# Kernel optimization log

Hardware: AMD Instinct MI355X
Metric: run time of the kernel (lower is better)

## Reference

```python
import jax, jax.numpy as jnp
import numpy as np

NUM_CLASSES = 80
STRIDES = (8, 16, 32)
PRE_TOP_K = 1000
KEEP_TOP_K = 100
IOU_THR = 0.65
SCORE_THR = 0.25
CLASS_OFFSET = 8192.0  # > max image coordinate, separates classes for batched NMS


def _make_priors_strides(featmap_sizes):
    # MlvlPointGenerator.grid_priors with offset=0 (RTMDet-style point priors)
    priors, strides = [], []
    for (h, w), s in zip(featmap_sizes, STRIDES):
        ys, xs = jnp.meshgrid(jnp.arange(h, dtype=jnp.float32) * s,
                              jnp.arange(w, dtype=jnp.float32) * s, indexing='ij')
        priors.append(jnp.stack([xs.reshape(-1), ys.reshape(-1)], axis=-1))
        strides.append(jnp.full((h * w,), float(s), dtype=jnp.float32))
    return jnp.concatenate(priors, 0), jnp.concatenate(strides, 0)


def _flatten(x, c):
    # [B, C, H, W] -> [B, H*W, c] matching permute(0,2,3,1).reshape
    b = x.shape[0]
    return jnp.transpose(x, (0, 2, 3, 1)).reshape(b, -1, c)


def _iou_matrix(boxes):
    # boxes [K, 4] x1y1x2y2 -> pairwise IoU [K, K]
    area = jnp.maximum(boxes[:, 2] - boxes[:, 0], 0.0) * jnp.maximum(boxes[:, 3] - boxes[:, 1], 0.0)
    lt = jnp.maximum(boxes[:, None, :2], boxes[None, :, :2])
    rb = jnp.minimum(boxes[:, None, 2:], boxes[None, :, 2:])
    wh = jnp.maximum(rb - lt, 0.0)
    inter = wh[..., 0] * wh[..., 1]
    return inter / jnp.maximum(area[:, None] + area[None, :] - inter, 1e-6)


def _nms_single(boxes, scores, labels):
    # boxes [N,4], scores [N] (max over classes), labels [N] int32
    valid = scores > SCORE_THR
    scores = jnp.where(valid, scores, 0.0)
    top_scores, idx = jax.lax.top_k(scores, PRE_TOP_K)  # pre_top_k filtering
    b = boxes[idx]
    lab = labels[idx]
    val = valid[idx]
    # class-aware NMS via coordinate offset per class (batched_nms trick)
    off_boxes = b + (lab.astype(b.dtype) * CLASS_OFFSET)[:, None]
    iou = _iou_matrix(off_boxes)

    def body(suppressed, i):
        keep_i = ~suppressed[i]
        suppressed = suppressed | (keep_i & (iou[i] > IOU_THR))
        suppressed = suppressed.at[i].set(~keep_i)
        return suppressed, keep_i

    _, keeps = jax.lax.scan(body, ~val, jnp.arange(PRE_TOP_K))
    final_scores = jnp.where(keeps, top_scores, 0.0)
    fs, fidx = jax.lax.top_k(final_scores, KEEP_TOP_K)
    dets = jnp.concatenate([b[fidx], fs[:, None]], axis=-1)  # [keep_top_k, 5]
    return dets, lab[fidx]


def setup_inputs() -> dict:
    key = jax.random.key(0)
    ks = jax.random.split(key, 6)
    B, C = 16, NUM_CLASSES
    return {
        'cls0': jax.random.normal(ks[0], (B, C, 80, 80), jnp.float32),
        'cls1': jax.random.normal(ks[1], (B, C, 40, 40), jnp.float32),
        'cls2': jax.random.normal(ks[2], (B, C, 20, 20), jnp.float32),
        'box0': jax.random.uniform(ks[3], (B, 4, 80, 80), jnp.float32),
        'box1': jax.random.uniform(ks[4], (B, 4, 40, 40), jnp.float32),
        'box2': jax.random.uniform(ks[5], (B, 4, 20, 20), jnp.float32),
    }


def reference(cls0, cls1, cls2, box0, box1, box2):
    featmap_sizes = [c.shape[2:] for c in (cls0, cls1, cls2)]
    priors, strides = _make_priors_strides(featmap_sizes)  # [A,2], [A]
    scores = jax.nn.sigmoid(
        jnp.concatenate([_flatten(c, NUM_CLASSES) for c in (cls0, cls1, cls2)], axis=1))  # [B,A,C]
    preds = jnp.concatenate([_flatten(b, 4) for b in (box0, box1, box2)], axis=1)  # [B,A,4]
    # rtmdet_bbox_decoder: distances * stride around point priors
    d = preds * strides[None, :, None]
    x1 = priors[None, :, 0] - d[..., 0]
    y1 = priors[None, :, 1] - d[..., 1]
    x2 = priors[None, :, 0] + d[..., 2]
    y2 = priors[None, :, 1] + d[..., 3]
    bboxes = jnp.stack([x1, y1, x2, y2], axis=-1)  # [B,A,4]
    max_scores = jnp.max(scores, axis=-1)
    labels = jnp.argmax(scores, axis=-1).astype(jnp.int32)
    dets, out_labels = jax.vmap(_nms_single)(bboxes, max_scores, labels)
    return dets, out_labels
```

## Files before the change

### kernel.cpp

```cpp
#include <hip/hip_runtime.h>
#include <math.h>
#include <stdint.h>

typedef unsigned long long u64;
typedef unsigned int u32;

#define NCLS 80
#define NA   8400
#define NB   16
#define PRE_K 1000
#define M_FAST 256


__global__ __launch_bounds__(256) void k_decode(
    const float* __restrict__ cls0, const float* __restrict__ cls1,
    const float* __restrict__ cls2, const float* __restrict__ box0,
    const float* __restrict__ box1, const float* __restrict__ box2,
    u64* __restrict__ f_keys, float4* __restrict__ boxes,
    int* __restrict__ labels)
{
    int pa = blockIdx.x * 256 + threadIdx.x;
    int b  = blockIdx.y;
    if (pa >= 4200) return;

    const float *clsp, *boxp;
    int Wd, s, HW, hw;
    if (pa < 3200)      { clsp = cls0; boxp = box0; Wd = 80; s = 8;  HW = 6400; hw = 2 * pa; }
    else if (pa < 4000) { clsp = cls1; boxp = box1; Wd = 40; s = 16; HW = 1600; hw = 2 * pa - 6400; }
    else                { clsp = cls2; boxp = box2; Wd = 20; s = 32; HW = 400;  hw = 2 * pa - 8000; }
    int a = 2 * pa;

    const float* cp = clsp + (size_t)b * NCLS * HW + hw;
    float2 v = *(const float2*)cp;
    float m0 = v.x, m1 = v.y;
    int lab0 = 0, lab1 = 0;
#pragma unroll 8
    for (int c = 1; c < NCLS; ++c) {
        float2 vv = *(const float2*)(cp + (size_t)c * HW);
        if (vv.x > m0) { m0 = vv.x; lab0 = c; }
        if (vv.y > m1) { m1 = vv.y; lab1 = c; }
    }
    double e0 = exp(-(double)m0), e1 = exp(-(double)m1);
    float sc0 = (float)(1.0 / (1.0 + e0));
    float sc1 = (float)(1.0 / (1.0 + e1));
    float sz0 = (sc0 > 0.25f) ? sc0 : 0.0f;
    float sz1 = (sc1 > 0.25f) ? sc1 : 0.0f;
    u64* fkp = f_keys + (size_t)b * NA + a;
    fkp[0] = ((u64)__float_as_uint(sz0) << 32) | (u64)(~(u32)a);
    fkp[1] = ((u64)__float_as_uint(sz1) << 32) | (u64)(~(u32)(a + 1));

    const float* bp = boxp + (size_t)b * 4 * HW + hw;
    float fs = (float)s;
    float2 q0 = *(const float2*)(bp);
    float2 q1 = *(const float2*)(bp + HW);
    float2 q2 = *(const float2*)(bp + 2 * HW);
    float2 q3 = *(const float2*)(bp + 3 * HW);
    float px = (float)((hw % Wd) * s);
    float py = (float)((hw / Wd) * s);
    float px1 = px + fs;
    boxes[(size_t)b * NA + a]     = make_float4(px  - q0.x * fs, py - q1.x * fs, px  + q2.x * fs, py + q3.x * fs);
    boxes[(size_t)b * NA + a + 1] = make_float4(px1 - q0.y * fs, py - q1.y * fs, px1 + q2.y * fs, py + q3.y * fs);
    int2 lt; lt.x = lab0; lt.y = lab1;
    *(int2*)(labels + (size_t)b * NA + a) = lt;
}

__device__ __forceinline__ u64 iou_bits(float4 A, float aar,
                                        const float4* __restrict__ bj,
                                        const float* __restrict__ aj, int jmax)
{
    u64 bits = 0;
    for (int jj = 0; jj < jmax; ++jj) {
        float4 Bx = bj[jj];
        float sab = aj[jj];
        float lx = fmaxf(A.x, Bx.x), ly = fmaxf(A.y, Bx.y);
        float rx = fminf(A.z, Bx.z), ry = fminf(A.w, Bx.w);
        float ww = fmaxf(__fsub_rn(rx, lx), 0.0f);
        float hh = fmaxf(__fsub_rn(ry, ly), 0.0f);
        float inter = __fmul_rn(ww, hh);
        float uni = __fsub_rn(__fadd_rn(aar, sab), inter);
        if (inter > 0.65f * fmaxf(uni, 1e-6f)) bits |= (1ull << jj);
    }
    return bits;
}

__global__ __launch_bounds__(1024, 1) void k_post(
    const u64* __restrict__ f_keys, const float4* __restrict__ boxes,
    const int* __restrict__ labels, u64* __restrict__ cand,
    float* __restrict__ out)
{
    __shared__ __align__(16) char shm[65536];
    __shared__ u32 wtot[16];
    __shared__ u32 s_total, s_B, s_kept;
    int tid = threadIdx.x, lane = tid & 63, wv = tid >> 6;
    int b = blockIdx.x;

    const u64* fk = f_keys + (size_t)b * NA;
    u64* cb = cand + (size_t)b * 1024;

    {
        u32* R  = (u32*)shm;
        u32* C  = (u32*)(shm + 16384);
        u64* BK = (u64*)(shm + 32768);

        for (int i = tid; i < 4096; i += 1024) { R[i] = 0; C[i] = 0; }
        __syncthreads();

        for (int i = tid; i < NA; i += 1024) {
            u32 sb = (u32)(fk[i] >> 32);
            if (sb) {
                int bin = (int)(sb >> 12) - 0x3E800;
                bin = max(0, min(bin, 4095));
                atomicAdd(&R[bin], 1u);
            }
        }
        __syncthreads();

        u32 h0 = R[4*tid], h1 = R[4*tid+1], h2 = R[4*tid+2], h3 = R[4*tid+3];
        u32 g = h0 + h1 + h2 + h3;
        u32 S = g;
#pragma unroll
        for (int off = 1; off < 64; off <<= 1) {
            u32 x = __shfl_down(S, off, 64);
            if (lane + off < 64) S += x;
        }
        if (lane == 0) wtot[wv] = S;
        __syncthreads();
        u32 wsuf = 0;
#pragma unroll
        for (int w = 0; w < 16; ++w) if (w > wv) wsuf += wtot[w];
        u32 above = (S - g) + wsuf;
        u32 r3 = h3 + above, r2 = h2 + r3, r1 = h1 + r2, r0 = h0 + r1;
        R[4*tid] = r0; R[4*tid+1] = r1; R[4*tid+2] = r2; R[4*tid+3] = r3;
        if (tid == 0) s_total = 0;
        __syncthreads();
        if (tid == 0) s_total = R[0];
        __syncthreads();
        u32 total = s_total;

        if (tid == 0 && total < PRE_K) s_B = 0;
#pragma unroll
        for (int k = 0; k < 4; ++k) {
            int bin = 4*tid + k;
            u32 Rb = R[bin];
            u32 Rn = (bin < 4095) ? R[bin + 1] : 0;
            if (Rb >= PRE_K && Rn < PRE_K) s_B = (u32)bin;
        }
        __syncthreads();
        u32 B = s_B;
        u32 Cv = R[B];

        if (Cv <= 4096) {
            for (int i = tid; i < NA; i += 1024) {
                u64 key = fk[i];
                u32 sb = (u32)(key >> 32);
                if (sb) {
                    int bin = (int)(sb >> 12) - 0x3E800;
                    bin = max(0, min(bin, 4095));
                    if ((u32)bin >= B) {
                        u32 base = (bin < 4095) ? R[bin + 1] : 0;
                        u32 off = atomicAdd(&C[bin], 1u);
                        BK[base + off] = key;
                    }
                }
            }
            __syncthreads();
            for (int s2 = tid; s2 < (int)Cv; s2 += 1024) {
                u64 key = BK[s2];
                u32 sb = (u32)(key >> 32);
                int bin = (int)(sb >> 12) - 0x3E800;
                bin = max(0, min(bin, 4095));
                u32 base = (bin < 4095) ? R[bin + 1] : 0;
                u32 n = R[bin] - base;
                u32 cnt = 0;
                for (u32 j = 0; j < n; ++j) cnt += (BK[base + j] > key) ? 1u : 0u;
                u32 rank = base + cnt;
                if (rank < PRE_K) cb[rank] = key;
            }
        } else {
            for (int i = tid; i < NA; i += 1024) {
                u64 key = fk[i];
                u32 sb = (u32)(key >> 32);
                if (!sb) continue;
                int bin = (int)(sb >> 12) - 0x3E800;
                bin = max(0, min(bin, 4095));
                if ((u32)bin < B) continue;
                u32 rank = 0;
                for (int j = 0; j < NA; ++j) rank += (fk[j] > key) ? 1u : 0u;
                if (rank < PRE_K) cb[rank] = key;
            }
        }
        for (int t2 = tid; (int)total + t2 < PRE_K; t2 += 1024)
            cb[total + t2] = (u64)(~(u32)t2);
        __syncthreads();
    }

    float4* sbox = (float4*)shm;
    float*  sar  = (float*)(shm + 16384);
    u64*    ck   = (u64*)(shm + 20480);
    u64*    mk   = (u64*)(shm + 28672);
    u64*    Ksh  = (u64*)(shm + 36864);
    int*    chgA = (int*)(shm + 37120);

    if (tid < PRE_K) {
        u64 key = cb[tid];
        ck[tid] = key;
        u32 a = ~(u32)key;
        float4 bx = boxes[(size_t)b * NA + a];
        float off = (float)labels[(size_t)b * NA + a] * 8192.0f;
        float x1 = bx.x + off, y1 = bx.y + off, x2 = bx.z + off, y2 = bx.w + off;
        sbox[tid] = make_float4(x1, y1, x2, y2);
        float w = fmaxf(__fsub_rn(x2, x1), 0.0f);
        float h = fmaxf(__fsub_rn(y2, y1), 0.0f);
        sar[tid] = __fmul_rn(w, h);
    }
    __syncthreads();

    {
        int i = tid & 255, w = tid >> 8;
        u64 bits = 0;
        int iw = i >> 6;
        if (w <= iw) {
            int jmax = (w < iw) ? 64 : (i & 63);
            bits = iou_bits(sbox[i], sar[i], sbox + w * 64, sar + w * 64, jmax);
        }
        mk[i * 4 + w] = bits;
    }
    __syncthreads();

    bool inr = tid < M_FAST;
    u64 key = (tid < PRE_K) ? ck[tid] : 0ull;
    bool valid = inr && ((u32)(key >> 32) != 0u);
    u64 rowm4[4];
#pragma unroll
    for (int k = 0; k < 4; ++k) rowm4[k] = inr ? mk[tid * 4 + k] : 0ull;

    u64 v0 = __ballot(valid);
    if (inr && lane == 0) Ksh[wv] = v0;
    if (tid < 32) chgA[tid] = 0;
    __syncthreads();

    int fin = 0;
    for (int it = 0; it < M_FAST + 2; ++it) {
        int p = it & 1;
        const u64* Kc = Ksh + p * 4;
        u64 kold = inr ? Kc[wv] : 0ull;
        u64 acc = 0;
#pragma unroll
        for (int k = 0; k < 4; ++k) acc |= rowm4[k] & Kc[k];
        bool kept = valid && (acc == 0ull);
        u64 nk = __ballot(kept);
        if (inr && lane == 0) {
            Ksh[(p ^ 1) * 4 + wv] = nk;
            if (nk != kold) chgA[it & 31] = 1;
        }
        __syncthreads();
        fin = p ^ 1;
        if (chgA[it & 31] == 0) break;
        if ((it & 31) == 31) {
            __syncthreads();
            if (tid < 32) chgA[tid] = 0;
            __syncthreads();
        }
    }
    const u64* Kf = Ksh + fin * 4;
    if (tid == 0) {
        u32 kt = 0;
#pragma unroll
        for (int k = 0; k < 4; ++k) kt += __popcll(Kf[k]);
        s_kept = kt;
    }
    __syncthreads();

    if (s_kept >= 100) {
        if (inr) {
            bool kept = (Kf[wv] >> lane) & 1ull;
            u64 low = (1ull << lane) - 1ull;
            int pc = 0;
#pragma unroll
            for (int k = 0; k < 4; ++k) {
                u64 lt = (k < wv) ? ~0ull : ((k == wv) ? low : 0ull);
                pc += __popcll(Kf[k] & lt);
            }
            if (kept && pc < 100) {
                u32 a = ~(u32)key;
                float4 bx = boxes[(size_t)b * NA + a];
                int lab = labels[(size_t)b * NA + a];
                float fsc = __uint_as_float((u32)(key >> 32));
                float* dr = out + (size_t)(b * 100 + pc) * 5;
                dr[0] = bx.x; dr[1] = bx.y; dr[2] = bx.z; dr[3] = bx.w; dr[4] = fsc;
                out[(size_t)NB * 100 * 5 + b * 100 + pc] = (float)lab;
            }
        }
        return;
    }

    {
        bool inrF = tid < PRE_K;
        u64 rowm[16];
#pragma unroll
        for (int k = 0; k < 16; ++k) rowm[k] = 0ull;
        if (inrF) {
            float4 A = sbox[tid];
            float aar = sar[tid];
            for (int k = 0; k <= wv; ++k) {
                int jmax = (k < wv) ? 64 : lane;
                rowm[k] = iou_bits(A, aar, sbox + k * 64, sar + k * 64, jmax);
            }
        }
        bool valid2 = inrF && ((u32)(key >> 32) != 0u);

        u64 vF = __ballot(valid2);
        if (lane == 0) Ksh[wv] = vF;
        if (tid < 32) chgA[tid] = 0;
        __syncthreads();

        int finF = 0;
        for (int it = 0; it < PRE_K + 2; ++it) {
            int p = it & 1;
            const u64* Kc = Ksh + p * 16;
            u64 kold = Kc[wv];
            u64 acc = 0;
#pragma unroll
            for (int k = 0; k < 16; ++k) acc |= rowm[k] & Kc[k];
            bool kept = valid2 && (acc == 0ull);
            u64 nk = __ballot(kept);
            if (lane == 0) {
                Ksh[(p ^ 1) * 16 + wv] = nk;
                if (nk != kold) chgA[it & 31] = 1;
            }
            __syncthreads();
            finF = p ^ 1;
            if (chgA[it & 31] == 0) break;
            if ((it & 31) == 31) {
                __syncthreads();
                if (tid < 32) chgA[tid] = 0;
                __syncthreads();
            }
        }
        const u64* Kf2 = Ksh + finF * 16;

        u64 low = (1ull << lane) - 1ull;
        int pc = 0, Kt = 0;
#pragma unroll
        for (int k = 0; k < 16; ++k) {
            u64 kk = Kf2[k];
            u64 lt = (k < wv) ? ~0ull : ((k == wv) ? low : 0ull);
            pc += __popcll(kk & lt);
            Kt += __popcll(kk);
        }
        if (inrF) {
            bool kept = (Kf2[wv] >> lane) & 1ull;
            int row = kept ? pc : (Kt + (tid - pc));
            if (row < 100) {
                u32 a = ~(u32)key;
                float4 bx = boxes[(size_t)b * NA + a];
                int lab = labels[(size_t)b * NA + a];
                float fsc = kept ? __uint_as_float((u32)(key >> 32)) : 0.0f;
                float* dr = out + (size_t)(b * 100 + row) * 5;
                dr[0] = bx.x; dr[1] = bx.y; dr[2] = bx.z; dr[3] = bx.w; dr[4] = fsc;
                out[(size_t)NB * 100 * 5 + b * 100 + row] = (float)lab;
            }
        }
    }
}

extern "C" void kernel_launch(void* const* d_in, const int* in_sizes, int n_in,
                              void* d_out, int out_size, void* d_ws, size_t ws_size,
                              hipStream_t stream) {
    const float* cls0 = (const float*)d_in[0];
    const float* cls1 = (const float*)d_in[1];
    const float* cls2 = (const float*)d_in[2];
    const float* box0 = (const float*)d_in[3];
    const float* box1 = (const float*)d_in[4];
    const float* box2 = (const float*)d_in[5];
    float* out = (float*)d_out;

    char* w = (char*)d_ws;
    u64*    f_keys = (u64*)(w);
    float4* boxes  = (float4*)(w + 1075200);
    int*    labels = (int*)(w + 3225600);
    u64*    cand   = (u64*)(w + 3763200);

    k_decode<<<dim3(17, NB), 256, 0, stream>>>(cls0, cls1, cls2, box0, box1, box2,
                                               f_keys, boxes, labels);
    k_post<<<NB, 1024, 0, stream>>>(f_keys, boxes, labels, cand, out);
}
```

Before: 110.5 us.

## Split class-max across four waves in decode and keep candidates in LDS

The decode kernel now gives each 64-point group four waves, each scanning 20 classes; partial maxima are reduced through shared memory, and box decoding moves to a separate wave. This launches four times as many blocks, so more memory requests are in flight at once. The post kernel preloads each image's keys into registers once instead of rereading global memory on every pass. It keeps the top-1000 candidate list in LDS rather than a global scratch buffer, and loads boxes beyond the first 256 only when the slow NMS path runs. The costs are more threads and an extra barrier in decode, plus more LDS and registers per block in the post kernel.

After: 106.6 us. -3.5%, faster.

```diff
diff --git a/kernel.cpp b/kernel.cpp
--- a/kernel.cpp
+++ b/kernel.cpp
@@ -19,49 +19,72 @@
     u64* __restrict__ f_keys, float4* __restrict__ boxes,
     int* __restrict__ labels)
 {
-    int pa = blockIdx.x * 256 + threadIdx.x;
+    __shared__ float pm0[3][64], pm1[3][64];
+    __shared__ int   pl0[3][64], pl1[3][64];
+
+    int t  = threadIdx.x & 63;
+    int q  = threadIdx.x >> 6;
+    int pa = blockIdx.x * 64 + t;
     int b  = blockIdx.y;
-    if (pa >= 4200) return;
-
-    const float *clsp, *boxp;
-    int Wd, s, HW, hw;
-    if (pa < 3200)      { clsp = cls0; boxp = box0; Wd = 80; s = 8;  HW = 6400; hw = 2 * pa; }
-    else if (pa < 4000) { clsp = cls1; boxp = box1; Wd = 40; s = 16; HW = 1600; hw = 2 * pa - 6400; }
-    else                { clsp = cls2; boxp = box2; Wd = 20; s = 32; HW = 400;  hw = 2 * pa - 8000; }
+    bool act = pa < 4200;
+
+    const float *clsp = cls0, *boxp = box0;
+    int Wd = 80, s = 8, HW = 6400, hw = 0;
+    float m0 = -1e30f, m1 = -1e30f;
+    int lab0 = q * 20, lab1 = q * 20;
+
+    if (act) {
+        if (pa < 3200)      { clsp = cls0; boxp = box0; Wd = 80; s = 8;  HW = 6400; hw = 2 * pa; }
+        else if (pa < 4000) { clsp = cls1; boxp = box1; Wd = 40; s = 16; HW = 1600; hw = 2 * pa - 6400; }
+        else                { clsp = cls2; boxp = box2; Wd = 20; s = 32; HW = 400;  hw = 2 * pa - 8000; }
+
+        const float* cp = clsp + (size_t)b * NCLS * HW + (size_t)(q * 20) * HW + hw;
+        float2 v = *(const float2*)cp;
+        m0 = v.x; m1 = v.y;
+#pragma unroll
+        for (int c = 1; c < 20; ++c) {
+            float2 vv = *(const float2*)(cp + (size_t)c * HW);
+            if (vv.x > m0) { m0 = vv.x; lab0 = q * 20 + c; }
+            if (vv.y > m1) { m1 = vv.y; lab1 = q * 20 + c; }
+        }
+        if (q > 0) {
+            pm0[q - 1][t] = m0; pl0[q - 1][t] = lab0;
+            pm1[q - 1][t] = m1; pl1[q - 1][t] = lab1;
+        }
+    }
+    __syncthreads();
+    if (!act) return;
     int a = 2 * pa;
 
-    const float* cp = clsp + (size_t)b * NCLS * HW + hw;
-    float2 v = *(const float2*)cp;
-    float m0 = v.x, m1 = v.y;
-    int lab0 = 0, lab1 = 0;
-#pragma unroll 8
-    for (int c = 1; c < NCLS; ++c) {
-        float2 vv = *(const float2*)(cp + (size_t)c * HW);
-        if (vv.x > m0) { m0 = vv.x; lab0 = c; }
-        if (vv.y > m1) { m1 = vv.y; lab1 = c; }
-    }
-    double e0 = exp(-(double)m0), e1 = exp(-(double)m1);
-    float sc0 = (float)(1.0 / (1.0 + e0));
-    float sc1 = (float)(1.0 / (1.0 + e1));
-    float sz0 = (sc0 > 0.25f) ? sc0 : 0.0f;
-    float sz1 = (sc1 > 0.25f) ? sc1 : 0.0f;
-    u64* fkp = f_keys + (size_t)b * NA + a;
-    fkp[0] = ((u64)__float_as_uint(sz0) << 32) | (u64)(~(u32)a);
-    fkp[1] = ((u64)__float_as_uint(sz1) << 32) | (u64)(~(u32)(a + 1));
-
-    const float* bp = boxp + (size_t)b * 4 * HW + hw;
-    float fs = (float)s;
-    float2 q0 = *(const float2*)(bp);
-    float2 q1 = *(const float2*)(bp + HW);
-    float2 q2 = *(const float2*)(bp + 2 * HW);
-    float2 q3 = *(const float2*)(bp + 3 * HW);
-    float px = (float)((hw % Wd) * s);
-    float py = (float)((hw / Wd) * s);
-    float px1 = px + fs;
-    boxes[(size_t)b * NA + a]     = make_float4(px  - q0.x * fs, py - q1.x * fs, px  + q2.x * fs, py + q3.x * fs);
-    boxes[(size_t)b * NA + a + 1] = make_float4(px1 - q0.y * fs, py - q1.y * fs, px1 + q2.y * fs, py + q3.y * fs);
-    int2 lt; lt.x = lab0; lt.y = lab1;
-    *(int2*)(labels + (size_t)b * NA + a) = lt;
+    if (q == 0) {
+#pragma unroll
+        for (int k = 0; k < 3; ++k) {
+            float a0 = pm0[k][t]; if (a0 > m0) { m0 = a0; lab0 = pl0[k][t]; }
+            float a1 = pm1[k][t]; if (a1 > m1) { m1 = a1; lab1 = pl1[k][t]; }
+        }
+        double e0 = exp(-(double)m0), e1 = exp(-(double)m1);
+        float sc0 = (float)(1.0 / (1.0 + e0));
+        float sc1 = (float)(1.0 / (1.0 + e1));
+        float sz0 = (sc0 > 0.25f) ? sc0 : 0.0f;
+        float sz1 = (sc1 > 0.25f) ? sc1 : 0.0f;
+        u64* fkp = f_keys + (size_t)b * NA + a;
+        fkp[0] = ((u64)__float_as_uint(sz0) << 32) | (u64)(~(u32)a);
+        fkp[1] = ((u64)__float_as_uint(sz1) << 32) | (u64)(~(u32)(a + 1));
+        int2 lt; lt.x = lab0; lt.y = lab1;
+        *(int2*)(labels + (size_t)b * NA + a) = lt;
+    } else if (q == 1) {
+        const float* bp = boxp + (size_t)b * 4 * HW + hw;
+        float fs = (float)s;
+        float2 q0v = *(const float2*)(bp);
+        float2 q1v = *(const float2*)(bp + HW);
+        float2 q2v = *(const float2*)(bp + 2 * HW);
+        float2 q3v = *(const float2*)(bp + 3 * HW);
+        float px = (float)((hw % Wd) * s);
+        float py = (float)((hw / Wd) * s);
+        float px1 = px + fs;
+        boxes[(size_t)b * NA + a]     = make_float4(px  - q0v.x * fs, py - q1v.x * fs, px  + q2v.x * fs, py + q3v.x * fs);
+        boxes[(size_t)b * NA + a + 1] = make_float4(px1 - q0v.y * fs, py - q1v.y * fs, px1 + q2v.y * fs, py + q3v.y * fs);
+    }
 }
 
 __device__ __forceinline__ u64 iou_bits(float4 A, float aar,
@@ -85,17 +108,23 @@
 
 __global__ __launch_bounds__(1024, 1) void k_post(
     const u64* __restrict__ f_keys, const float4* __restrict__ boxes,
-    const int* __restrict__ labels, u64* __restrict__ cand,
-    float* __restrict__ out)
+    const int* __restrict__ labels, float* __restrict__ out)
 {
     __shared__ __align__(16) char shm[65536];
+    __shared__ __align__(16) u64 cbs[1024];
     __shared__ u32 wtot[16];
     __shared__ u32 s_total, s_B, s_kept;
     int tid = threadIdx.x, lane = tid & 63, wv = tid >> 6;
     int b = blockIdx.x;
 
     const u64* fk = f_keys + (size_t)b * NA;
-    u64* cb = cand + (size_t)b * 1024;
+
+    u64 kr[9];
+#pragma unroll
+    for (int k = 0; k < 9; ++k) {
+        int i = tid + k * 1024;
+        kr[k] = (i < NA) ? fk[i] : 0ull;
+    }
 
     {
         u32* R  = (u32*)shm;
@@ -105,8 +134,9 @@
         for (int i = tid; i < 4096; i += 1024) { R[i] = 0; C[i] = 0; }
         __syncthreads();
 
-        for (int i = tid; i < NA; i += 1024) {
-            u32 sb = (u32)(fk[i] >> 32);
+#pragma unroll
+        for (int k = 0; k < 9; ++k) {
+            u32 sb = (u32)(kr[k] >> 32);
             if (sb) {
                 int bin = (int)(sb >> 12) - 0x3E800;
                 bin = max(0, min(bin, 4095));
@@ -150,8 +180,9 @@
         u32 Cv = R[B];
 
         if (Cv <= 4096) {
-            for (int i = tid; i < NA; i += 1024) {
-                u64 key = fk[i];
+#pragma unroll
+            for (int k = 0; k < 9; ++k) {
+                u64 key = kr[k];
                 u32 sb = (u32)(key >> 32);
                 if (sb) {
                     int bin = (int)(sb >> 12) - 0x3E800;
@@ -174,7 +205,7 @@
                 u32 cnt = 0;
                 for (u32 j = 0; j < n; ++j) cnt += (BK[base + j] > key) ? 1u : 0u;
                 u32 rank = base + cnt;
-                if (rank < PRE_K) cb[rank] = key;
+                if (rank < PRE_K) cbs[rank] = key;
             }
         } else {
             for (int i = tid; i < NA; i += 1024) {
@@ -186,24 +217,22 @@
                 if ((u32)bin < B) continue;
                 u32 rank = 0;
                 for (int j = 0; j < NA; ++j) rank += (fk[j] > key) ? 1u : 0u;
-                if (rank < PRE_K) cb[rank] = key;
+                if (rank < PRE_K) cbs[rank] = key;
             }
         }
         for (int t2 = tid; (int)total + t2 < PRE_K; t2 += 1024)
-            cb[total + t2] = (u64)(~(u32)t2);
+            cbs[total + t2] = (u64)(~(u32)t2);
         __syncthreads();
     }
 
     float4* sbox = (float4*)shm;
     float*  sar  = (float*)(shm + 16384);
-    u64*    ck   = (u64*)(shm + 20480);
-    u64*    mk   = (u64*)(shm + 28672);
-    u64*    Ksh  = (u64*)(shm + 36864);
-    int*    chgA = (int*)(shm + 37120);
-
-    if (tid < PRE_K) {
-        u64 key = cb[tid];
-        ck[tid] = key;
+    u64*    mk   = (u64*)(shm + 20480);
+    u64*    Ksh  = (u64*)(shm + 28672);
+    int*    chgA = (int*)(shm + 28928);
+
+    if (tid < M_FAST) {
+        u64 key = cbs[tid];
         u32 a = ~(u32)key;
         float4 bx = boxes[(size_t)b * NA + a];
         float off = (float)labels[(size_t)b * NA + a] * 8192.0f;
@@ -228,7 +257,7 @@
     __syncthreads();
 
     bool inr = tid < M_FAST;
-    u64 key = (tid < PRE_K) ? ck[tid] : 0ull;
+    u64 key = (tid < PRE_K) ? cbs[tid] : 0ull;
     bool valid = inr && ((u32)(key >> 32) != 0u);
     u64 rowm4[4];
 #pragma unroll
@@ -295,6 +324,19 @@
     }
 
     {
+        if (tid >= M_FAST && tid < PRE_K) {
+            u64 kk = cbs[tid];
+            u32 a = ~(u32)kk;
+            float4 bx = boxes[(size_t)b * NA + a];
+            float off = (float)labels[(size_t)b * NA + a] * 8192.0f;
+            float x1 = bx.x + off, y1 = bx.y + off, x2 = bx.z + off, y2 = bx.w + off;
+            sbox[tid] = make_float4(x1, y1, x2, y2);
+            float w = fmaxf(__fsub_rn(x2, x1), 0.0f);
+            float h = fmaxf(__fsub_rn(y2, y1), 0.0f);
+            sar[tid] = __fmul_rn(w, h);
+        }
+        __syncthreads();
+
         bool inrF = tid < PRE_K;
         u64 rowm[16];
 #pragma unroll
@@ -379,9 +421,8 @@
     u64*    f_keys = (u64*)(w);
     float4* boxes  = (float4*)(w + 1075200);
     int*    labels = (int*)(w + 3225600);
-    u64*    cand   = (u64*)(w + 3763200);
-
-    k_decode<<<dim3(17, NB), 256, 0, stream>>>(cls0, cls1, cls2, box0, box1, box2,
+
+    k_decode<<<dim3(66, NB), 256, 0, stream>>>(cls0, cls1, cls2, box0, box1, box2,
                                                f_keys, boxes, labels);
-    k_post<<<NB, 1024, 0, stream>>>(f_keys, boxes, labels, cand, out);
+    k_post<<<NB, 1024, 0, stream>>>(f_keys, boxes, labels, out);
 }
```
